# Optimization experiments

Hardware: AMD Instinct MI355X
Metric: run time of the kernel (lower is better)

Reference implementation:

```python
import jax, jax.numpy as jnp
import numpy as np

CK, CV, CS = 8, 120, 64          # key / value / spatial-basis channels
NUM_AGENTS, NQ_PER = 4, 4        # queries chunked per agent; chunk(a,4) hard-codes NQ_PER=4
HID = 256                        # lstm_hidden_size
NA = 18                          # num_actions
U = 8                            # Fourier freqs; CS = U*U = 64
MLP_W = 512                      # q/a mlp hidden width


def spatial_basis(h, w):
    # fixed (h, w, CS) cos-product Fourier basis (SpatialBasis buffer)
    ph = jnp.arange(1, h + 1, dtype=jnp.float32)[:, None] * jnp.ones((1, w), jnp.float32) * (np.pi / h)
    pw = jnp.ones((h, 1), jnp.float32) * jnp.arange(1, w + 1, dtype=jnp.float32)[None, :] * (np.pi / w)
    u = jnp.arange(1, U + 1, dtype=jnp.float32)
    ca = jnp.cos(ph[..., None] * u)   # (h, w, U)
    cb = jnp.cos(pw[..., None] * u)   # (h, w, U)
    return jnp.einsum('hwu,hwv->hwuv', ca, cb).reshape(h, w, U * U)


def mlp3(x, w0, b0, w1, b1, w2, b2):
    # build_mlp with 2 relu hidden layers + identity output
    x = jax.nn.relu(x @ w0 + b0)
    x = jax.nn.relu(x @ w1 + b1)
    return x @ w2 + b2


def lstm_cell(x, h, c, w_ih, w_hh, b_ih, b_hh):
    gates = x @ w_ih.T + b_ih + h @ w_hh.T + b_hh
    i, f, g, o = jnp.split(gates, 4, axis=1)
    c2 = jax.nn.sigmoid(f) * c + jax.nn.sigmoid(i) * jnp.tanh(g)
    return jax.nn.sigmoid(o) * jnp.tanh(c2), c2


def setup_inputs() -> dict:
    key = jax.random.key(0)
    ks = jax.random.split(key, 24)
    n, h, w = 128, 64, 64
    s = 0.02
    nq = NUM_AGENTS * NQ_PER
    q_out = nq * (CK + CS)                       # 1152
    a_in = NQ_PER * (CK + 2 * CS + CV) + 2       # 1026
    r = lambda k, shp: jax.random.normal(k, shp, jnp.float32)
    return {
        'x': r(ks[0], (n, h, w, CK + CV)),
        'c': 1,
        'r_prev': r(ks[1], (n,)),
        'a_prev': r(ks[2], (n,)),
        'prev_hidden': r(ks[3], (n, HID)),
        'prev_cell': r(ks[4], (n, HID)),
        'q_w0': r(ks[5], (HID, MLP_W)) * s, 'q_b0': jnp.zeros((MLP_W,), jnp.float32),
        'q_w1': r(ks[6], (MLP_W, MLP_W)) * s, 'q_b1': jnp.zeros((MLP_W,), jnp.float32),
        'q_w2': r(ks[7], (MLP_W, q_out)) * s, 'q_b2': jnp.zeros((q_out,), jnp.float32),
        'a_w0': r(ks[8], (a_in, MLP_W)) * s, 'a_b0': jnp.zeros((MLP_W,), jnp.float32),
        'a_w1': r(ks[9], (MLP_W, MLP_W)) * s, 'a_b1': jnp.zeros((MLP_W,), jnp.float32),
        'a_w2': r(ks[10], (MLP_W, HID)) * s, 'a_b2': jnp.zeros((HID,), jnp.float32),
        'w_ih': r(ks[11], (4 * HID, HID)) * s, 'w_hh': r(ks[12], (4 * HID, HID)) * s,
        'b_ih': jnp.zeros((4 * HID,), jnp.float32), 'b_hh': jnp.zeros((4 * HID,), jnp.float32),
        'p_w': r(ks[13], (HID, NA)) * s, 'p_b': jnp.zeros((NA,), jnp.float32),
        'v_w': r(ks[14], (HID, NA)) * s, 'v_b': jnp.zeros((NA,), jnp.float32),
    }


def reference(x, c, r_prev, a_prev, prev_hidden, prev_cell,
              q_w0, q_b0, q_w1, q_b1, q_w2, q_b2,
              a_w0, a_b0, a_w1, a_b1, a_w2, a_b2,
              w_ih, w_hh, b_ih, b_hh, p_w, p_b, v_w, v_b):
    n, h, w, _ = x.shape
    S = spatial_basis(h, w)
    Sb = jnp.broadcast_to(S, (n, h, w, CS))
    K = jnp.concatenate([x[..., :CK], Sb], axis=-1)   # (n,h,w,CK+CS)
    V = jnp.concatenate([x[..., CK:], Sb], axis=-1)   # (n,h,w,CV+CS)
    # queries from previous hidden state, take agent c's chunk
    Q = mlp3(prev_hidden, q_w0, q_b0, q_w1, q_b1, q_w2, q_b2)
    Q = Q.reshape(n, NUM_AGENTS * NQ_PER, CK + CS)[:, c * NQ_PER:(c + 1) * NQ_PER, :]  # (n,4,CK+CS)
    # spatial QK attention with softmax over the h*w grid
    A = jnp.einsum('nhwd,nqd->nhwq', K, Q)            # (n,h,w,4)
    A = jax.nn.softmax(A.reshape(n, h * w, NQ_PER), axis=1).reshape(n, h, w, NQ_PER)
    a = jnp.einsum('nhwq,nhwd->nqd', A, V)            # (n,4,CV+CS)
    # concat answers + queries + prev reward/action scalars
    answer = jnp.concatenate([a.reshape(n, -1), Q.reshape(n, -1),
                              r_prev[:, None], a_prev[:, None]], axis=1)  # (n,1026)
    answer = mlp3(answer, a_w0, a_b0, a_w1, a_b1, a_w2, a_b2)             # (n,HID)
    hN, _cN = lstm_cell(answer, prev_hidden, prev_cell, w_ih, w_hh, b_ih, b_hh)
    logits = hN @ p_w + p_b
    values = hN @ v_w + v_b
    return logits, values
```

## Files before the change

### kernel.cpp

```cpp
#include <hip/hip_runtime.h>
#include <math.h>

#define NTOT   128
#define NPOS   4096
#define PVCH   8
#define PVLEN  512
#define LCH    4
#define LCLEN  1024

__global__ __launch_bounds__(256) void k_gemm(
    const float* __restrict__ Ad, const float* __restrict__ pA,
    const float* __restrict__ biasA, int nzA, int reluA,
    const float* __restrict__ pvR, const float* __restrict__ scl,
    const float* __restrict__ W, float* __restrict__ pbuf,
    int N, int K, int ldw, int gkc, const int* __restrict__ cptr, int cmul) {
  __shared__ float Xs[4][128];
  const int t  = threadIdx.x;
  const int j  = blockIdx.x * 256 + t;
  const int m0 = blockIdx.y * 4;
  const int k0 = blockIdx.z * gkc;
  const int klen = min(gkc, K - k0);
  const int coff = cptr[0] * cmul;

  for (int idx = t; idx < 4 * klen; idx += 256) {
    int mi = idx / klen;
    int kk = idx - mi * klen;
    int col = k0 + kk;
    float s;
    if (Ad) {
      bool pv = false;
      int q = 0, d = 0;
      if (pvR && col < 736) {
        q = col / 184; d = col - q * 184;
        pv = (d < 120);
      }
      if (pv) {
        const size_t eo = (size_t)(m0 + mi) * 480 + q * 120 + d;
        const float* scp = scl + (size_t)(m0 + mi) * 16 + q;
        float p0 = pvR[(size_t)(0 * NTOT) * 480 + eo];
        float p1 = pvR[(size_t)(1 * NTOT) * 480 + eo];
        float p2 = pvR[(size_t)(2 * NTOT) * 480 + eo];
        float p3 = pvR[(size_t)(3 * NTOT) * 480 + eo];
        float p4 = pvR[(size_t)(4 * NTOT) * 480 + eo];
        float p5 = pvR[(size_t)(5 * NTOT) * 480 + eo];
        float p6 = pvR[(size_t)(6 * NTOT) * 480 + eo];
        float p7 = pvR[(size_t)(7 * NTOT) * 480 + eo];
        s = scp[0] * (p0 + p1) + scp[4] * (p2 + p3)
          + scp[8] * (p4 + p5) + scp[12] * (p6 + p7);
      } else {
        s = Ad[(size_t)(m0 + mi) * K + col];
      }
    } else {
      float s0 = biasA[col], s1 = 0.f, s2 = 0.f, s3 = 0.f;
      int z = 0;
      for (; z + 4 <= nzA; z += 4) {
        s0 += pA[((size_t)(z + 0) * NTOT + m0 + mi) * K + col];
        s1 += pA[((size_t)(z + 1) * NTOT + m0 + mi) * K + col];
        s2 += pA[((size_t)(z + 2) * NTOT + m0 + mi) * K + col];
        s3 += pA[((size_t)(z + 3) * NTOT + m0 + mi) * K + col];
      }
      for (; z < nzA; ++z) s0 += pA[((size_t)z * NTOT + m0 + mi) * K + col];
      s = (s0 + s1) + (s2 + s3);
      if (reluA) s = fmaxf(s, 0.f);
    }
    Xs[mi][kk] = s;
  }
  __syncthreads();

  if (j < N) {
    float acc[4];
#pragma unroll
    for (int mi = 0; mi < 4; ++mi) acc[mi] = 0.f;
    const float* wp = W + (size_t)k0 * ldw + coff + j;
#pragma unroll 16
    for (int kk = 0; kk < klen; ++kk) {
      float wv = wp[(size_t)kk * ldw];
#pragma unroll
      for (int mi = 0; mi < 4; ++mi) acc[mi] = fmaf(Xs[mi][kk], wv, acc[mi]);
    }
    float* op = pbuf + ((size_t)blockIdx.z * NTOT + m0) * N + j;
#pragma unroll
    for (int mi = 0; mi < 4; ++mi) op[(size_t)mi * N] = acc[mi];
  }
}

__global__ __launch_bounds__(256) void k_logit_part(
    const float* __restrict__ x, const float* __restrict__ pQ,
    const float* __restrict__ q_b2, const int* __restrict__ cptr,
    const float* __restrict__ r_prev, const float* __restrict__ a_prev,
    float* __restrict__ Pw, float* __restrict__ stats,
    float* __restrict__ rowSumP, float* __restrict__ ans) {
  const int ck = blockIdx.x;
  const int n  = blockIdx.y;
  const int t  = threadIdx.x;
  const int wave = t >> 6, lane = t & 63;

  __shared__ float Qs[4][72];
  __shared__ float ct[64][8];
  __shared__ float cbQ[4 * 576];
  __shared__ float4 wlds[LCLEN];
  __shared__ float red[4][4];
  __shared__ float mfin[4], lfin[4];

  const float PI64 = 3.14159265358979323846f / 64.f;

  {
    const int coff = cptr[0] * 288;
    for (int idx = t; idx < 288; idx += 256) {
      float s = q_b2[coff + idx];
#pragma unroll
      for (int z = 0; z < 8; ++z) s += pQ[((size_t)z * NTOT + n) * 288 + idx];
      Qs[idx / 72][idx % 72] = s;
    }
  }
  for (int e = t; e < 512; e += 256) {
    int i = e >> 3, u = e & 7;
    ct[i][u] = cosf((float)((i + 1) * (u + 1)) * PI64);
  }
  __syncthreads();

  for (int e = t; e < 2048; e += 256) {
    int q = e >> 9, j = (e >> 3) & 63, u = e & 7;
    float s = 0.f;
#pragma unroll
    for (int v = 0; v < 8; ++v) s += ct[j][v] * Qs[q][8 + u * 8 + v];
    cbQ[q * 576 + j * 9 + u] = s;
  }
  __syncthreads();

  const int base = ck * LCLEN;
  const float* xp = x + (size_t)n * NPOS * 128;

  float lmax[4] = {-1e30f, -1e30f, -1e30f, -1e30f};
#pragma unroll
  for (int r = 0; r < 4; ++r) {
    const int local = r * 256 + t;
    const int pos = base + local;
    const int i = ck * 16 + r * 4 + wave;
    const float4* xr = reinterpret_cast<const float4*>(xp + (size_t)pos * 128);
    float4 xa = xr[0], xb = xr[1];
    float lg[4];
#pragma unroll
    for (int q = 0; q < 4; ++q) {
      float s = xa.x * Qs[q][0] + xa.y * Qs[q][1] + xa.z * Qs[q][2] + xa.w * Qs[q][3]
              + xb.x * Qs[q][4] + xb.y * Qs[q][5] + xb.z * Qs[q][6] + xb.w * Qs[q][7];
      const float* cq = cbQ + q * 576 + lane * 9;
      float s2 = 0.f;
#pragma unroll
      for (int u = 0; u < 8; ++u) s2 += ct[i][u] * cq[u];
      lg[q] = s + s2;
      lmax[q] = fmaxf(lmax[q], lg[q]);
    }
    wlds[local] = make_float4(lg[0], lg[1], lg[2], lg[3]);
  }

#pragma unroll
  for (int off = 32; off; off >>= 1)
#pragma unroll
    for (int q = 0; q < 4; ++q) lmax[q] = fmaxf(lmax[q], __shfl_xor(lmax[q], off));
  if (lane == 0)
#pragma unroll
    for (int q = 0; q < 4; ++q) red[q][wave] = lmax[q];
  __syncthreads();
  if (t < 4) mfin[t] = fmaxf(fmaxf(red[t][0], red[t][1]), fmaxf(red[t][2], red[t][3]));
  __syncthreads();

  float4* Pw4 = reinterpret_cast<float4*>(Pw) + (size_t)n * NPOS + base;
  float lsum[4] = {0.f, 0.f, 0.f, 0.f};
#pragma unroll
  for (int r = 0; r < 4; ++r) {
    const int local = r * 256 + t;
    float4 w = wlds[local];
    w.x = __expf(w.x - mfin[0]);
    w.y = __expf(w.y - mfin[1]);
    w.z = __expf(w.z - mfin[2]);
    w.w = __expf(w.w - mfin[3]);
    wlds[local] = w;
    Pw4[local] = w;
    lsum[0] += w.x; lsum[1] += w.y; lsum[2] += w.z; lsum[3] += w.w;
  }
#pragma unroll
  for (int off = 32; off; off >>= 1)
#pragma unroll
    for (int q = 0; q < 4; ++q) lsum[q] += __shfl_xor(lsum[q], off);
  if (lane == 0)
#pragma unroll
    for (int q = 0; q < 4; ++q) red[q][wave] = lsum[q];
  __syncthreads();
  if (t < 4) {
    lfin[t] = red[t][0] + red[t][1] + red[t][2] + red[t][3];
    stats[((size_t)n * LCH + ck) * 8 + t] = mfin[t];
    stats[((size_t)n * LCH + ck) * 8 + 4 + t] = lfin[t];
  }
  __syncthreads();

  for (int o = t; o < 512; o += 256) {
    int i = o >> 5, q = (o >> 3) & 3, v = o & 7;
    const float* wb = reinterpret_cast<const float*>(&wlds[i * 64]) + q;
    float s0 = 0.f, s1 = 0.f, s2 = 0.f, s3 = 0.f;
#pragma unroll 8
    for (int j = 0; j < 64; j += 4) {
      s0 += wb[(j + 0) * 4] * ct[j + 0][v];
      s1 += wb[(j + 1) * 4] * ct[j + 1][v];
      s2 += wb[(j + 2) * 4] * ct[j + 2][v];
      s3 += wb[(j + 3) * 4] * ct[j + 3][v];
    }
    rowSumP[(((size_t)n * LCH + ck) * 16 + i) * 32 + q * 8 + v] = (s0 + s1) + (s2 + s3);
  }

  if (ck == 0) {
    float* ap = ans + (size_t)n * 1026;
    for (int idx = t; idx < 288; idx += 256) ap[736 + idx] = Qs[idx / 72][idx % 72];
    if (t == 0) { ap[1024] = r_prev[n]; ap[1025] = a_prev[n]; }
  }
}

__global__ __launch_bounds__(256) void k_fin(
    const float* __restrict__ stats, const float* __restrict__ rowSumP,
    float* __restrict__ scales, float* __restrict__ ans) {
  const int n = blockIdx.x, t = threadIdx.x;
  __shared__ float ct[64][8];
  __shared__ float sc[LCH][4];
  const float PI64 = 3.14159265358979323846f / 64.f;

  for (int e = t; e < 512; e += 256) {
    int i = e >> 3, u = e & 7;
    ct[i][u] = cosf((float)((i + 1) * (u + 1)) * PI64);
  }
  if (t < 16) {
    const int q = t & 3, ck = t >> 2;
    float M = -1e30f;
#pragma unroll
    for (int c = 0; c < LCH; ++c) M = fmaxf(M, stats[((size_t)n * LCH + c) * 8 + q]);
    float L = 0.f;
#pragma unroll
    for (int c = 0; c < LCH; ++c)
      L += stats[((size_t)n * LCH + c) * 8 + 4 + q] *
           __expf(stats[((size_t)n * LCH + c) * 8 + q] - M);
    sc[ck][q] = __expf(stats[((size_t)n * LCH + ck) * 8 + q] - M) / L;
  }
  __syncthreads();
  if (t < 16) scales[(size_t)n * 16 + t] = sc[t >> 2][t & 3];

  {
    const int q = t >> 6, uv = t & 63, u = uv >> 3, v = uv & 7;
    float s = 0.f;
#pragma unroll
    for (int ck = 0; ck < LCH; ++ck) {
      float ss = 0.f;
#pragma unroll 4
      for (int i = 0; i < 16; ++i)
        ss += ct[ck * 16 + i][u] *
              rowSumP[(((size_t)n * LCH + ck) * 16 + i) * 32 + q * 8 + v];
      s += sc[ck][q] * ss;
    }
    ans[(size_t)n * 1026 + q * 184 + 120 + uv] = s;
  }
}

__global__ __launch_bounds__(256, 4) void k_pv(
    const float* __restrict__ x, const float* __restrict__ Pw,
    float* __restrict__ pvp) {
  const int n = blockIdx.y, ck = blockIdx.x;
  const int t = threadIdx.x, wave = t >> 6, lane = t & 63;
  __shared__ float4 wl[PVLEN];
  __shared__ __align__(16) float part[4][4][120];

  const int base = ck * PVLEN;
  {
    const float4* src = reinterpret_cast<const float4*>(Pw) + (size_t)n * NPOS + base;
    wl[t] = src[t];
    wl[t + 256] = src[t + 256];
  }
  __syncthreads();

  const int xl = (lane < 60) ? lane : 59;
  const float* vb = x + ((size_t)n * NPOS + base + wave * 128) * 128 + 8 + 2 * xl;

  float ax0[4] = {0.f, 0.f, 0.f, 0.f};
  float ax1[4] = {0.f, 0.f, 0.f, 0.f};
#pragma unroll
  for (int b = 0; b < 8; ++b) {
    float2 v0  = *reinterpret_cast<const float2*>(vb + (size_t)(b * 16 + 0)  * 128);
    float2 v1  = *reinterpret_cast<const float2*>(vb + (size_t)(b * 16 + 1)  * 128);
    float2 v2  = *reinterpret_cast<const float2*>(vb + (size_t)(b * 16 + 2)  * 128);
    float2 v3  = *reinterpret_cast<const float2*>(vb + (size_t)(b * 16 + 3)  * 128);
    float2 v4  = *reinterpret_cast<const float2*>(vb + (size_t)(b * 16 + 4)  * 128);
    float2 v5  = *reinterpret_cast<const float2*>(vb + (size_t)(b * 16 + 5)  * 128);
    float2 v6  = *reinterpret_cast<const float2*>(vb + (size_t)(b * 16 + 6)  * 128);
    float2 v7  = *reinterpret_cast<const float2*>(vb + (size_t)(b * 16 + 7)  * 128);
    float2 v8  = *reinterpret_cast<const float2*>(vb + (size_t)(b * 16 + 8)  * 128);
    float2 v9  = *reinterpret_cast<const float2*>(vb + (size_t)(b * 16 + 9)  * 128);
    float2 v10 = *reinterpret_cast<const float2*>(vb + (size_t)(b * 16 + 10) * 128);
    float2 v11 = *reinterpret_cast<const float2*>(vb + (size_t)(b * 16 + 11) * 128);
    float2 v12 = *reinterpret_cast<const float2*>(vb + (size_t)(b * 16 + 12) * 128);
    float2 v13 = *reinterpret_cast<const float2*>(vb + (size_t)(b * 16 + 13) * 128);
    float2 v14 = *reinterpret_cast<const float2*>(vb + (size_t)(b * 16 + 14) * 128);
    float2 v15 = *reinterpret_cast<const float2*>(vb + (size_t)(b * 16 + 15) * 128);
#define ACC(VV, II)                                                              \
    {                                                                            \
      float4 w = wl[wave * 128 + b * 16 + II];                                   \
      ax0[0] += w.x * VV.x; ax1[0] += w.x * VV.y;                                \
      ax0[1] += w.y * VV.x; ax1[1] += w.y * VV.y;                                \
      ax0[2] += w.z * VV.x; ax1[2] += w.z * VV.y;                                \
      ax0[3] += w.w * VV.x; ax1[3] += w.w * VV.y;                                \
    }
    ACC(v0, 0)  ACC(v1, 1)  ACC(v2, 2)  ACC(v3, 3)
    ACC(v4, 4)  ACC(v5, 5)  ACC(v6, 6)  ACC(v7, 7)
    ACC(v8, 8)  ACC(v9, 9)  ACC(v10, 10) ACC(v11, 11)
    ACC(v12, 12) ACC(v13, 13) ACC(v14, 14) ACC(v15, 15)
#undef ACC
  }
  if (lane < 60) {
#pragma unroll
    for (int q = 0; q < 4; ++q)
      *reinterpret_cast<float2*>(&part[wave][q][2 * lane]) = make_float2(ax0[q], ax1[q]);
  }
  __syncthreads();

  float* op = pvp + ((size_t)ck * NTOT + n) * 480;
  for (int idx = t; idx < 480; idx += 256) {
    const int q = idx / 120, d = idx - q * 120;
    op[idx] = (part[0][q][d] + part[1][q][d]) + (part[2][q][d] + part[3][q][d]);
  }
}

__global__ __launch_bounds__(256) void k_gates(
    const float* __restrict__ pA, const float* __restrict__ biasA,
    const float* __restrict__ hp,
    const float* __restrict__ w_ih, const float* __restrict__ w_hh,
    const float* __restrict__ b_ih, const float* __restrict__ b_hh,
    float* __restrict__ gbuf) {
  const int t = threadIdx.x;
  const int n0 = blockIdx.x * 2;
  const int r0 = blockIdx.y * 64;
  __shared__ float xs[2][256], hs[2][256];
  __shared__ float red[64][4][5];
#pragma unroll
  for (int s = 0; s < 2; ++s) {
    float v0 = biasA[t], v1 = 0.f, v2 = 0.f, v3 = 0.f;
#pragma unroll
    for (int z = 0; z < 8; z += 4) {
      v0 += pA[((size_t)(z + 0) * NTOT + n0 + s) * 256 + t];
      v1 += pA[((size_t)(z + 1) * NTOT + n0 + s) * 256 + t];
      v2 += pA[((size_t)(z + 2) * NTOT + n0 + s) * 256 + t];
      v3 += pA[((size_t)(z + 3) * NTOT + n0 + s) * 256 + t];
    }
    xs[s][t] = (v0 + v1) + (v2 + v3);
    hs[s][t] = hp[(size_t)(n0 + s) * 256 + t];
  }
  __syncthreads();
  const int r = t >> 2, kq = t & 3;
  const int row = r0 + r;
  const float4* wi = reinterpret_cast<const float4*>(w_ih + (size_t)row * 256 + kq * 64);
  const float4* wh = reinterpret_cast<const float4*>(w_hh + (size_t)row * 256 + kq * 64);
  float s00 = 0.f, s01 = 0.f, s10 = 0.f, s11 = 0.f;
#pragma unroll
  for (int i = 0; i < 16; ++i) {
    float4 a = wi[i], b = wh[i];
    const int k4 = kq * 64 + i * 4;
    s00 += a.x * xs[0][k4] + a.y * xs[0][k4 + 1] + a.z * xs[0][k4 + 2] + a.w * xs[0][k4 + 3];
    s01 += a.x * xs[1][k4] + a.y * xs[1][k4 + 1] + a.z * xs[1][k4 + 2] + a.w * xs[1][k4 + 3];
    s10 += b.x * hs[0][k4] + b.y * hs[0][k4 + 1] + b.z * hs[0][k4 + 2] + b.w * hs[0][k4 + 3];
    s11 += b.x * hs[1][k4] + b.y * hs[1][k4 + 1] + b.z * hs[1][k4 + 2] + b.w * hs[1][k4 + 3];
  }
  red[r][kq][0] = s00; red[r][kq][1] = s01; red[r][kq][2] = s10; red[r][kq][3] = s11;
  __syncthreads();
  if (t < 128) {
    const int rr = t >> 1, s = t & 1;
    float g = b_ih[r0 + rr] + b_hh[r0 + rr];
#pragma unroll
    for (int k = 0; k < 4; ++k) g += red[rr][k][s] + red[rr][k][2 + s];
    gbuf[(size_t)(n0 + s) * 1024 + r0 + rr] = g;
  }
}

__global__ __launch_bounds__(256) void k_lstm2(
    const float* __restrict__ gbuf, const float* __restrict__ cp,
    const float* __restrict__ p_w, const float* __restrict__ p_b,
    const float* __restrict__ v_w, const float* __restrict__ v_b,
    float* __restrict__ out) {
  const int t = threadIdx.x;
  const int n0 = blockIdx.x * 2;
  __shared__ float h2[2][256];
#pragma unroll
  for (int s = 0; s < 2; ++s) {
    const size_t gb = (size_t)(n0 + s) * 1024;
    float gi = gbuf[gb + t], gf = gbuf[gb + 256 + t];
    float gg = gbuf[gb + 512 + t], go = gbuf[gb + 768 + t];
    float si = 1.f / (1.f + __expf(-gi));
    float sf = 1.f / (1.f + __expf(-gf));
    float so = 1.f / (1.f + __expf(-go));
    float c2 = sf * cp[(size_t)(n0 + s) * 256 + t] + si * tanhf(gg);
    h2[s][t] = so * tanhf(c2);
  }
  __syncthreads();
  if (t < 72) {
    const int si = t / 36, r = t % 36, iv = r / 18, j = r % 18;
    const float* W = iv ? v_w : p_w;
    const float* B = iv ? v_b : p_b;
    float s = B[j];
#pragma unroll 8
    for (int k = 0; k < 256; ++k) s += h2[si][k] * W[k * 18 + j];
    out[(size_t)iv * (NTOT * 18) + (size_t)(n0 + si) * 18 + j] = s;
  }
}

extern "C" void kernel_launch(void* const* d_in, const int* in_sizes, int n_in,
                              void* d_out, int out_size, void* d_ws, size_t ws_size,
                              hipStream_t stream) {
  const float* x      = (const float*)d_in[0];
  const int*   cptr   = (const int*)d_in[1];
  const float* r_prev = (const float*)d_in[2];
  const float* a_prev = (const float*)d_in[3];
  const float* hprev  = (const float*)d_in[4];
  const float* cprev  = (const float*)d_in[5];
  const float* q_w0 = (const float*)d_in[6];
  const float* q_b0 = (const float*)d_in[7];
  const float* q_w1 = (const float*)d_in[8];
  const float* q_b1 = (const float*)d_in[9];
  const float* q_w2 = (const float*)d_in[10];
  const float* q_b2 = (const float*)d_in[11];
  const float* a_w0 = (const float*)d_in[12];
  const float* a_b0 = (const float*)d_in[13];
  const float* a_w1 = (const float*)d_in[14];
  const float* a_b1 = (const float*)d_in[15];
  const float* a_w2 = (const float*)d_in[16];
  const float* a_b2 = (const float*)d_in[17];
  const float* w_ih = (const float*)d_in[18];
  const float* w_hh = (const float*)d_in[19];
  const float* b_ih = (const float*)d_in[20];
  const float* b_hh = (const float*)d_in[21];
  const float* p_w  = (const float*)d_in[22];
  const float* p_b  = (const float*)d_in[23];
  const float* v_w  = (const float*)d_in[24];
  const float* v_b  = (const float*)d_in[25];
  float* out = (float*)d_out;
  float* ws  = (float*)d_ws;

  float* pQ   = ws;
  float* pb1  = pQ   + 294912;
  float* pb2  = pb1  + 589824;
  float* pb3  = pb2  + 524288;
  float* Pw   = pb3  + 262144;
  float* pvp  = Pw   + 2097152;
  float* ans  = pvp  + 491520;
  float* gbuf = ans  + 131328;
  float* stats= gbuf + 131072;
  float* rsum = stats+ 4096;
  float* scl  = rsum + 262144;

  k_gemm<<<dim3(2, 32, 4), 256, 0, stream>>>(hprev, nullptr, nullptr, 0, 0, nullptr, nullptr,
                                             q_w0, pb1, 512, 256, 512, 64, cptr, 0);
  k_gemm<<<dim3(2, 32, 8), 256, 0, stream>>>(nullptr, pb1, q_b0, 4, 1, nullptr, nullptr,
                                             q_w1, pb2, 512, 512, 512, 64, cptr, 0);
  k_gemm<<<dim3(2, 32, 8), 256, 0, stream>>>(nullptr, pb2, q_b1, 8, 1, nullptr, nullptr,
                                             q_w2, pQ, 288, 512, 1152, 64, cptr, 288);

  k_logit_part<<<dim3(LCH, NTOT), 256, 0, stream>>>(x, pQ, q_b2, cptr, r_prev, a_prev,
                                                    Pw, stats, rsum, ans);
  k_pv<<<dim3(PVCH, NTOT), 256, 0, stream>>>(x, Pw, pvp);
  k_fin<<<NTOT, 256, 0, stream>>>(stats, rsum, scl, ans);

  k_gemm<<<dim3(2, 32, 9), 256, 0, stream>>>(ans, nullptr, nullptr, 0, 0, pvp, scl,
                                             a_w0, pb1, 512, 1026, 512, 128, cptr, 0);
  k_gemm<<<dim3(2, 32, 8), 256, 0, stream>>>(nullptr, pb1, a_b0, 9, 1, nullptr, nullptr,
                                             a_w1, pb2, 512, 512, 512, 64, cptr, 0);
  k_gemm<<<dim3(1, 32, 8), 256, 0, stream>>>(nullptr, pb2, a_b1, 8, 1, nullptr, nullptr,
                                             a_w2, pb3, 256, 512, 256, 64, cptr, 0);

  k_gates<<<dim3(64, 16), 256, 0, stream>>>(pb3, a_b2, hprev, w_ih, w_hh, b_ih, b_hh, gbuf);
  k_lstm2<<<64, 256, 0, stream>>>(gbuf, cprev, p_w, p_b, v_w, v_b, out);
}
```

Before: 143.4 us.

## Fuse logit softmax and PV accumulation into one split-softmax attention kernel

Merges the logit/partial-softmax kernel and the PV kernel into a single k_attn kernel over 16 chunks of 256 positions per sample. The unnormalized exp weights now stay in shared memory instead of being written to and re-read from a global Pw buffer. The per-chunk rescaling of the PV partials moves from the a_w0 GEMM's input loader into k_fin, which now writes the full answer vector, so the GEMM reads a plain input. The cost is more blocks, 16-way partial buffers and stats, and a heavier reduction in k_fin.

Result: slower. 205.5 us (+43.3%).

```diff
diff --git a/kernel.cpp b/kernel.cpp
--- a/kernel.cpp
+++ b/kernel.cpp
@@ -3,15 +3,12 @@
 
 #define NTOT   128
 #define NPOS   4096
-#define PVCH   8
-#define PVLEN  512
-#define LCH    4
-#define LCLEN  1024
+#define ACH    16
+#define ACLEN  256
 
 __global__ __launch_bounds__(256) void k_gemm(
     const float* __restrict__ Ad, const float* __restrict__ pA,
     const float* __restrict__ biasA, int nzA, int reluA,
-    const float* __restrict__ pvR, const float* __restrict__ scl,
     const float* __restrict__ W, float* __restrict__ pbuf,
     int N, int K, int ldw, int gkc, const int* __restrict__ cptr, int cmul) {
   __shared__ float Xs[4][128];
@@ -28,28 +25,7 @@
     int col = k0 + kk;
     float s;
     if (Ad) {
-      bool pv = false;
-      int q = 0, d = 0;
-      if (pvR && col < 736) {
-        q = col / 184; d = col - q * 184;
-        pv = (d < 120);
-      }
-      if (pv) {
-        const size_t eo = (size_t)(m0 + mi) * 480 + q * 120 + d;
-        const float* scp = scl + (size_t)(m0 + mi) * 16 + q;
-        float p0 = pvR[(size_t)(0 * NTOT) * 480 + eo];
-        float p1 = pvR[(size_t)(1 * NTOT) * 480 + eo];
-        float p2 = pvR[(size_t)(2 * NTOT) * 480 + eo];
-        float p3 = pvR[(size_t)(3 * NTOT) * 480 + eo];
-        float p4 = pvR[(size_t)(4 * NTOT) * 480 + eo];
-        float p5 = pvR[(size_t)(5 * NTOT) * 480 + eo];
-        float p6 = pvR[(size_t)(6 * NTOT) * 480 + eo];
-        float p7 = pvR[(size_t)(7 * NTOT) * 480 + eo];
-        s = scp[0] * (p0 + p1) + scp[4] * (p2 + p3)
-          + scp[8] * (p4 + p5) + scp[12] * (p6 + p7);
-      } else {
-        s = Ad[(size_t)(m0 + mi) * K + col];
-      }
+      s = Ad[(size_t)(m0 + mi) * K + col];
     } else {
       float s0 = biasA[col], s1 = 0.f, s2 = 0.f, s3 = 0.f;
       int z = 0;
@@ -84,11 +60,11 @@
   }
 }
 
-__global__ __launch_bounds__(256) void k_logit_part(
+__global__ __launch_bounds__(256, 4) void k_attn(
     const float* __restrict__ x, const float* __restrict__ pQ,
     const float* __restrict__ q_b2, const int* __restrict__ cptr,
     const float* __restrict__ r_prev, const float* __restrict__ a_prev,
-    float* __restrict__ Pw, float* __restrict__ stats,
+    float* __restrict__ pvp, float* __restrict__ stats,
     float* __restrict__ rowSumP, float* __restrict__ ans) {
   const int ck = blockIdx.x;
   const int n  = blockIdx.y;
@@ -97,10 +73,12 @@
 
   __shared__ float Qs[4][72];
   __shared__ float ct[64][8];
-  __shared__ float cbQ[4 * 576];
-  __shared__ float4 wlds[LCLEN];
+  __shared__ float4 wlds[ACLEN];
   __shared__ float red[4][4];
   __shared__ float mfin[4], lfin[4];
+  __shared__ __align__(16) float uni[2304];
+  float* cbQ = uni;
+  float (*part)[4][120] = reinterpret_cast<float (*)[4][120]>(uni);
 
   const float PI64 = 3.14159265358979323846f / 64.f;
 
@@ -128,15 +106,12 @@
   }
   __syncthreads();
 
-  const int base = ck * LCLEN;
+  const int base = ck * ACLEN;
   const float* xp = x + (size_t)n * NPOS * 128;
 
-  float lmax[4] = {-1e30f, -1e30f, -1e30f, -1e30f};
-#pragma unroll
-  for (int r = 0; r < 4; ++r) {
-    const int local = r * 256 + t;
-    const int pos = base + local;
-    const int i = ck * 16 + r * 4 + wave;
+  {
+    const int pos = base + t;
+    const int irow = ck * 4 + wave;
     const float4* xr = reinterpret_cast<const float4*>(xp + (size_t)pos * 128);
     float4 xa = xr[0], xb = xr[1];
     float lg[4];
@@ -147,140 +122,57 @@
       const float* cq = cbQ + q * 576 + lane * 9;
       float s2 = 0.f;
 #pragma unroll
-      for (int u = 0; u < 8; ++u) s2 += ct[i][u] * cq[u];
+      for (int u = 0; u < 8; ++u) s2 += ct[irow][u] * cq[u];
       lg[q] = s + s2;
-      lmax[q] = fmaxf(lmax[q], lg[q]);
-    }
-    wlds[local] = make_float4(lg[0], lg[1], lg[2], lg[3]);
-  }
-
-#pragma unroll
-  for (int off = 32; off; off >>= 1)
-#pragma unroll
-    for (int q = 0; q < 4; ++q) lmax[q] = fmaxf(lmax[q], __shfl_xor(lmax[q], off));
-  if (lane == 0)
-#pragma unroll
-    for (int q = 0; q < 4; ++q) red[q][wave] = lmax[q];
+    }
+    wlds[t] = make_float4(lg[0], lg[1], lg[2], lg[3]);
+
+    float lmax[4];
+#pragma unroll
+    for (int q = 0; q < 4; ++q) lmax[q] = lg[q];
+#pragma unroll
+    for (int off = 32; off; off >>= 1)
+#pragma unroll
+      for (int q = 0; q < 4; ++q) lmax[q] = fmaxf(lmax[q], __shfl_xor(lmax[q], off));
+    if (lane == 0)
+#pragma unroll
+      for (int q = 0; q < 4; ++q) red[q][wave] = lmax[q];
+  }
   __syncthreads();
   if (t < 4) mfin[t] = fmaxf(fmaxf(red[t][0], red[t][1]), fmaxf(red[t][2], red[t][3]));
   __syncthreads();
 
-  float4* Pw4 = reinterpret_cast<float4*>(Pw) + (size_t)n * NPOS + base;
-  float lsum[4] = {0.f, 0.f, 0.f, 0.f};
-#pragma unroll
-  for (int r = 0; r < 4; ++r) {
-    const int local = r * 256 + t;
-    float4 w = wlds[local];
-    w.x = __expf(w.x - mfin[0]);
-    w.y = __expf(w.y - mfin[1]);
-    w.z = __expf(w.z - mfin[2]);
-    w.w = __expf(w.w - mfin[3]);
-    wlds[local] = w;
-    Pw4[local] = w;
-    lsum[0] += w.x; lsum[1] += w.y; lsum[2] += w.z; lsum[3] += w.w;
-  }
-#pragma unroll
-  for (int off = 32; off; off >>= 1)
-#pragma unroll
-    for (int q = 0; q < 4; ++q) lsum[q] += __shfl_xor(lsum[q], off);
-  if (lane == 0)
-#pragma unroll
-    for (int q = 0; q < 4; ++q) red[q][wave] = lsum[q];
+  {
+    float4 wv = wlds[t];
+    wv.x = __expf(wv.x - mfin[0]);
+    wv.y = __expf(wv.y - mfin[1]);
+    wv.z = __expf(wv.z - mfin[2]);
+    wv.w = __expf(wv.w - mfin[3]);
+    wlds[t] = wv;
+    float lsum[4] = {wv.x, wv.y, wv.z, wv.w};
+#pragma unroll
+    for (int off = 32; off; off >>= 1)
+#pragma unroll
+      for (int q = 0; q < 4; ++q) lsum[q] += __shfl_xor(lsum[q], off);
+    if (lane == 0)
+#pragma unroll
+      for (int q = 0; q < 4; ++q) red[q][wave] = lsum[q];
+  }
   __syncthreads();
   if (t < 4) {
     lfin[t] = red[t][0] + red[t][1] + red[t][2] + red[t][3];
-    stats[((size_t)n * LCH + ck) * 8 + t] = mfin[t];
-    stats[((size_t)n * LCH + ck) * 8 + 4 + t] = lfin[t];
-  }
-  __syncthreads();
-
-  for (int o = t; o < 512; o += 256) {
-    int i = o >> 5, q = (o >> 3) & 3, v = o & 7;
-    const float* wb = reinterpret_cast<const float*>(&wlds[i * 64]) + q;
-    float s0 = 0.f, s1 = 0.f, s2 = 0.f, s3 = 0.f;
-#pragma unroll 8
-    for (int j = 0; j < 64; j += 4) {
-      s0 += wb[(j + 0) * 4] * ct[j + 0][v];
-      s1 += wb[(j + 1) * 4] * ct[j + 1][v];
-      s2 += wb[(j + 2) * 4] * ct[j + 2][v];
-      s3 += wb[(j + 3) * 4] * ct[j + 3][v];
-    }
-    rowSumP[(((size_t)n * LCH + ck) * 16 + i) * 32 + q * 8 + v] = (s0 + s1) + (s2 + s3);
-  }
-
-  if (ck == 0) {
-    float* ap = ans + (size_t)n * 1026;
-    for (int idx = t; idx < 288; idx += 256) ap[736 + idx] = Qs[idx / 72][idx % 72];
-    if (t == 0) { ap[1024] = r_prev[n]; ap[1025] = a_prev[n]; }
-  }
-}
-
-__global__ __launch_bounds__(256) void k_fin(
-    const float* __restrict__ stats, const float* __restrict__ rowSumP,
-    float* __restrict__ scales, float* __restrict__ ans) {
-  const int n = blockIdx.x, t = threadIdx.x;
-  __shared__ float ct[64][8];
-  __shared__ float sc[LCH][4];
-  const float PI64 = 3.14159265358979323846f / 64.f;
-
-  for (int e = t; e < 512; e += 256) {
-    int i = e >> 3, u = e & 7;
-    ct[i][u] = cosf((float)((i + 1) * (u + 1)) * PI64);
-  }
-  if (t < 16) {
-    const int q = t & 3, ck = t >> 2;
-    float M = -1e30f;
-#pragma unroll
-    for (int c = 0; c < LCH; ++c) M = fmaxf(M, stats[((size_t)n * LCH + c) * 8 + q]);
-    float L = 0.f;
-#pragma unroll
-    for (int c = 0; c < LCH; ++c)
-      L += stats[((size_t)n * LCH + c) * 8 + 4 + q] *
-           __expf(stats[((size_t)n * LCH + c) * 8 + q] - M);
-    sc[ck][q] = __expf(stats[((size_t)n * LCH + ck) * 8 + q] - M) / L;
-  }
-  __syncthreads();
-  if (t < 16) scales[(size_t)n * 16 + t] = sc[t >> 2][t & 3];
-
-  {
-    const int q = t >> 6, uv = t & 63, u = uv >> 3, v = uv & 7;
-    float s = 0.f;
-#pragma unroll
-    for (int ck = 0; ck < LCH; ++ck) {
-      float ss = 0.f;
-#pragma unroll 4
-      for (int i = 0; i < 16; ++i)
-        ss += ct[ck * 16 + i][u] *
-              rowSumP[(((size_t)n * LCH + ck) * 16 + i) * 32 + q * 8 + v];
-      s += sc[ck][q] * ss;
-    }
-    ans[(size_t)n * 1026 + q * 184 + 120 + uv] = s;
-  }
-}
-
-__global__ __launch_bounds__(256, 4) void k_pv(
-    const float* __restrict__ x, const float* __restrict__ Pw,
-    float* __restrict__ pvp) {
-  const int n = blockIdx.y, ck = blockIdx.x;
-  const int t = threadIdx.x, wave = t >> 6, lane = t & 63;
-  __shared__ float4 wl[PVLEN];
-  __shared__ __align__(16) float part[4][4][120];
-
-  const int base = ck * PVLEN;
-  {
-    const float4* src = reinterpret_cast<const float4*>(Pw) + (size_t)n * NPOS + base;
-    wl[t] = src[t];
-    wl[t + 256] = src[t + 256];
+    stats[((size_t)n * ACH + ck) * 8 + t] = mfin[t];
+    stats[((size_t)n * ACH + ck) * 8 + 4 + t] = lfin[t];
   }
   __syncthreads();
 
   const int xl = (lane < 60) ? lane : 59;
-  const float* vb = x + ((size_t)n * NPOS + base + wave * 128) * 128 + 8 + 2 * xl;
+  const float* vb = xp + (size_t)(base + wave * 64) * 128 + 8 + 2 * xl;
 
   float ax0[4] = {0.f, 0.f, 0.f, 0.f};
   float ax1[4] = {0.f, 0.f, 0.f, 0.f};
 #pragma unroll
-  for (int b = 0; b < 8; ++b) {
+  for (int b = 0; b < 4; ++b) {
     float2 v0  = *reinterpret_cast<const float2*>(vb + (size_t)(b * 16 + 0)  * 128);
     float2 v1  = *reinterpret_cast<const float2*>(vb + (size_t)(b * 16 + 1)  * 128);
     float2 v2  = *reinterpret_cast<const float2*>(vb + (size_t)(b * 16 + 2)  * 128);
@@ -299,7 +191,7 @@
     float2 v15 = *reinterpret_cast<const float2*>(vb + (size_t)(b * 16 + 15) * 128);
 #define ACC(VV, II)                                                              \
     {                                                                            \
-      float4 w = wl[wave * 128 + b * 16 + II];                                   \
+      float4 w = wlds[wave * 64 + b * 16 + II];                                  \
       ax0[0] += w.x * VV.x; ax1[0] += w.x * VV.y;                                \
       ax0[1] += w.y * VV.x; ax1[1] += w.y * VV.y;                                \
       ax0[2] += w.z * VV.x; ax1[2] += w.z * VV.y;                                \
@@ -318,10 +210,83 @@
   }
   __syncthreads();
 
-  float* op = pvp + ((size_t)ck * NTOT + n) * 480;
+  {
+    float* op = pvp + ((size_t)ck * NTOT + n) * 480;
+    for (int idx = t; idx < 480; idx += 256) {
+      const int q = idx / 120, d = idx - q * 120;
+      op[idx] = (part[0][q][d] + part[1][q][d]) + (part[2][q][d] + part[3][q][d]);
+    }
+  }
+
+  if (t < 128) {
+    int i = t >> 5, q = (t >> 3) & 3, v = t & 7;
+    const float* wb = reinterpret_cast<const float*>(&wlds[i * 64]) + q;
+    float s0 = 0.f, s1 = 0.f, s2 = 0.f, s3 = 0.f;
+#pragma unroll 8
+    for (int j = 0; j < 64; j += 4) {
+      s0 += wb[(j + 0) * 4] * ct[j + 0][v];
+      s1 += wb[(j + 1) * 4] * ct[j + 1][v];
+      s2 += wb[(j + 2) * 4] * ct[j + 2][v];
+      s3 += wb[(j + 3) * 4] * ct[j + 3][v];
+    }
+    rowSumP[(((size_t)n * ACH + ck) * 4 + i) * 32 + q * 8 + v] = (s0 + s1) + (s2 + s3);
+  }
+
+  if (ck == 0) {
+    float* ap = ans + (size_t)n * 1026;
+    for (int idx = t; idx < 288; idx += 256) ap[736 + idx] = Qs[idx / 72][idx % 72];
+    if (t == 0) { ap[1024] = r_prev[n]; ap[1025] = a_prev[n]; }
+  }
+}
+
+__global__ __launch_bounds__(256) void k_fin(
+    const float* __restrict__ stats, const float* __restrict__ rowSumP,
+    const float* __restrict__ pvp, float* __restrict__ ans) {
+  const int n = blockIdx.x, t = threadIdx.x;
+  __shared__ float ct[64][8];
+  __shared__ float sc[ACH][4];
+  const float PI64 = 3.14159265358979323846f / 64.f;
+
+  for (int e = t; e < 512; e += 256) {
+    int i = e >> 3, u = e & 7;
+    ct[i][u] = cosf((float)((i + 1) * (u + 1)) * PI64);
+  }
+  if (t < 64) {
+    const int ck = t >> 2, q = t & 3;
+    float M = -1e30f;
+#pragma unroll
+    for (int c = 0; c < ACH; ++c) M = fmaxf(M, stats[((size_t)n * ACH + c) * 8 + q]);
+    float L = 0.f;
+#pragma unroll
+    for (int c = 0; c < ACH; ++c)
+      L += stats[((size_t)n * ACH + c) * 8 + 4 + q] *
+           __expf(stats[((size_t)n * ACH + c) * 8 + q] - M);
+    sc[ck][q] = __expf(stats[((size_t)n * ACH + ck) * 8 + q] - M) / L;
+  }
+  __syncthreads();
+
+  float* ap = ans + (size_t)n * 1026;
   for (int idx = t; idx < 480; idx += 256) {
     const int q = idx / 120, d = idx - q * 120;
-    op[idx] = (part[0][q][d] + part[1][q][d]) + (part[2][q][d] + part[3][q][d]);
+    float s = 0.f;
+#pragma unroll
+    for (int ck = 0; ck < ACH; ++ck)
+      s += sc[ck][q] * pvp[((size_t)ck * NTOT + n) * 480 + q * 120 + d];
+    ap[q * 184 + d] = s;
+  }
+  {
+    const int q = t >> 6, uv = t & 63, u = uv >> 3, v = uv & 7;
+    float s = 0.f;
+#pragma unroll
+    for (int ck = 0; ck < ACH; ++ck) {
+      float ss = 0.f;
+#pragma unroll
+      for (int i = 0; i < 4; ++i)
+        ss += ct[ck * 4 + i][u] *
+              rowSumP[(((size_t)n * ACH + ck) * 4 + i) * 32 + q * 8 + v];
+      s += sc[ck][q] * ss;
+    }
+    ap[q * 184 + 120 + uv] = s;
   }
 }
 
@@ -442,31 +407,28 @@
   float* pb1  = pQ   + 294912;
   float* pb2  = pb1  + 589824;
   float* pb3  = pb2  + 524288;
-  float* Pw   = pb3  + 262144;
-  float* pvp  = Pw   + 2097152;
-  float* ans  = pvp  + 491520;
+  float* pvp  = pb3  + 262144;
+  float* ans  = pvp  + 983040;
   float* gbuf = ans  + 131328;
   float* stats= gbuf + 131072;
-  float* rsum = stats+ 4096;
-  float* scl  = rsum + 262144;
-
-  k_gemm<<<dim3(2, 32, 4), 256, 0, stream>>>(hprev, nullptr, nullptr, 0, 0, nullptr, nullptr,
+  float* rsum = stats+ 16384;
+
+  k_gemm<<<dim3(2, 32, 4), 256, 0, stream>>>(hprev, nullptr, nullptr, 0, 0,
                                              q_w0, pb1, 512, 256, 512, 64, cptr, 0);
-  k_gemm<<<dim3(2, 32, 8), 256, 0, stream>>>(nullptr, pb1, q_b0, 4, 1, nullptr, nullptr,
+  k_gemm<<<dim3(2, 32, 8), 256, 0, stream>>>(nullptr, pb1, q_b0, 4, 1,
                                              q_w1, pb2, 512, 512, 512, 64, cptr, 0);
-  k_gemm<<<dim3(2, 32, 8), 256, 0, stream>>>(nullptr, pb2, q_b1, 8, 1, nullptr, nullptr,
+  k_gemm<<<dim3(2, 32, 8), 256, 0, stream>>>(nullptr, pb2, q_b1, 8, 1,
                                              q_w2, pQ, 288, 512, 1152, 64, cptr, 288);
 
-  k_logit_part<<<dim3(LCH, NTOT), 256, 0, stream>>>(x, pQ, q_b2, cptr, r_prev, a_prev,
-                                                    Pw, stats, rsum, ans);
-  k_pv<<<dim3(PVCH, NTOT), 256, 0, stream>>>(x, Pw, pvp);
-  k_fin<<<NTOT, 256, 0, stream>>>(stats, rsum, scl, ans);
-
-  k_gemm<<<dim3(2, 32, 9), 256, 0, stream>>>(ans, nullptr, nullptr, 0, 0, pvp, scl,
+  k_attn<<<dim3(ACH, NTOT), 256, 0, stream>>>(x, pQ, q_b2, cptr, r_prev, a_prev,
+                                              pvp, stats, rsum, ans);
+  k_fin<<<NTOT, 256, 0, stream>>>(stats, rsum, pvp, ans);
+
+  k_gemm<<<dim3(2, 32, 9), 256, 0, stream>>>(ans, nullptr, nullptr, 0, 0,
                                              a_w0, pb1, 512, 1026, 512, 128, cptr, 0);
-  k_gemm<<<dim3(2, 32, 8), 256, 0, stream>>>(nullptr, pb1, a_b0, 9, 1, nullptr, nullptr,
+  k_gemm<<<dim3(2, 32, 8), 256, 0, stream>>>(nullptr, pb1, a_b0, 9, 1,
                                              a_w1, pb2, 512, 512, 512, 64, cptr, 0);
-  k_gemm<<<dim3(1, 32, 8), 256, 0, stream>>>(nullptr, pb2, a_b1, 8, 1, nullptr, nullptr,
+  k_gemm<<<dim3(1, 32, 8), 256, 0, stream>>>(nullptr, pb2, a_b1, 8, 1,
                                              a_w2, pb3, 256, 512, 256, 64, cptr, 0);
 
   k_gates<<<dim3(64, 16), 256, 0, stream>>>(pb3, a_b2, hprev, w_ih, w_hh, b_ih, b_hh, gbuf);
```
